# Kernel tuning notes

Hardware: AMD Instinct MI355X
Metric: run time of the kernel (lower is better)

The kernel has to match this reference:

```python
import jax, jax.numpy as jnp
import numpy as np

N, M, DZ, DX, HEADS = 8192, 128, 128, 128, 4


def setup_inputs() -> dict:
    key = jax.random.key(0)
    k1, k2, k3 = jax.random.split(key, 3)
    z = jax.random.normal(k1, (N, DZ), dtype=jnp.float32)
    x = jax.random.normal(k2, (DX, M), dtype=jnp.float32)
    # MLP([input_size, heads]) -> single Linear(DZ+DX, HEADS) + final_act
    W = jax.random.normal(k3, (DZ + DX, HEADS), dtype=jnp.float32) * (1.0 / np.sqrt(DZ + DX))
    b = jnp.zeros((HEADS,), dtype=jnp.float32)
    return {"z": z, "x": x, "W": W, "b": b}


def reference(z, x, W, b):
    # Original: cat([repeat_interleave(z[:,None], M, 1), x.T.repeat(N,1,1)], -1) @ W + b
    # Fused equivalent: split W into the z-part and x-part and broadcast-add.
    dz = z.shape[1]
    zW = jnp.einsum('nd,dh->nh', z, W[:dz])        # [N, H]
    xW = jnp.einsum('dm,dh->mh', x, W[dz:])        # [M, H] (x.T @ W2)
    out = zW[:, None, :] + xW[None, :, :] + b      # [N, M, H]
    return jax.nn.relu(out)
```

## Files before the change

### kernel.cpp

```cpp
#include <hip/hip_runtime.h>
#include <hip/hip_bf16.h>


using bf16 = __hip_bfloat16;

union F4 { float4 v; float f[4]; };

__device__ __forceinline__ int sw(int r) { return r + (r >> 3); }

__global__ void __launch_bounds__(256) gam_fused(
    const float* __restrict__ z, const float* __restrict__ x,
    const float* __restrict__ W, const float* __restrict__ b,
    float* __restrict__ out)
{
    __shared__ float4 Wf[292];
    __shared__ float4 tpart[2][128];
    __shared__ float4 tvec[128];
    __shared__ float4 zw[32];

    const int t   = threadIdx.x;
    const int blk = blockIdx.x;

    const float4* zp = (const float4*)(z + (size_t)blk * 32 * 128);
    F4 a0, a1, a2, a3;
    a0.v = zp[t];
    a1.v = zp[t + 256];
    a2.v = zp[t + 512];
    a3.v = zp[t + 768];

    Wf[sw(t)] = ((const float4*)W)[t];
    __syncthreads();

    {
        const int m    = t & 127;
        const int half = t >> 7;
        const float* xp = x + (size_t)(half * 64) * 128 + m;
        float4 acc = make_float4(0.f, 0.f, 0.f, 0.f);
#pragma unroll
        for (int dd = 0; dd < 64; ++dd) {
            float  xv = xp[dd * 128];
            float4 w  = Wf[sw(128 + half * 64 + dd)];
            acc.x = fmaf(xv, w.x, acc.x);
            acc.y = fmaf(xv, w.y, acc.y);
            acc.z = fmaf(xv, w.z, acc.z);
            acc.w = fmaf(xv, w.w, acc.w);
        }
        tpart[half][m] = acc;
    }

    {
        const int d0 = (t & 31) * 4;
        float4 p0 = make_float4(0.f,0.f,0.f,0.f);
        float4 p1 = make_float4(0.f,0.f,0.f,0.f);
        float4 p2 = make_float4(0.f,0.f,0.f,0.f);
        float4 p3 = make_float4(0.f,0.f,0.f,0.f);
#pragma unroll
        for (int j = 0; j < 4; ++j) {
            float4 w = Wf[sw(d0 + j)];
            p0.x = fmaf(a0.f[j], w.x, p0.x); p0.y = fmaf(a0.f[j], w.y, p0.y);
            p0.z = fmaf(a0.f[j], w.z, p0.z); p0.w = fmaf(a0.f[j], w.w, p0.w);
            p1.x = fmaf(a1.f[j], w.x, p1.x); p1.y = fmaf(a1.f[j], w.y, p1.y);
            p1.z = fmaf(a1.f[j], w.z, p1.z); p1.w = fmaf(a1.f[j], w.w, p1.w);
            p2.x = fmaf(a2.f[j], w.x, p2.x); p2.y = fmaf(a2.f[j], w.y, p2.y);
            p2.z = fmaf(a2.f[j], w.z, p2.z); p2.w = fmaf(a2.f[j], w.w, p2.w);
            p3.x = fmaf(a3.f[j], w.x, p3.x); p3.y = fmaf(a3.f[j], w.y, p3.y);
            p3.z = fmaf(a3.f[j], w.z, p3.z); p3.w = fmaf(a3.f[j], w.w, p3.w);
        }
#pragma unroll
        for (int off = 16; off; off >>= 1) {
            p0.x += __shfl_xor(p0.x, off); p0.y += __shfl_xor(p0.y, off);
            p0.z += __shfl_xor(p0.z, off); p0.w += __shfl_xor(p0.w, off);
            p1.x += __shfl_xor(p1.x, off); p1.y += __shfl_xor(p1.y, off);
            p1.z += __shfl_xor(p1.z, off); p1.w += __shfl_xor(p1.w, off);
            p2.x += __shfl_xor(p2.x, off); p2.y += __shfl_xor(p2.y, off);
            p2.z += __shfl_xor(p2.z, off); p2.w += __shfl_xor(p2.w, off);
            p3.x += __shfl_xor(p3.x, off); p3.y += __shfl_xor(p3.y, off);
            p3.z += __shfl_xor(p3.z, off); p3.w += __shfl_xor(p3.w, off);
        }
        if ((t & 31) == 0) {
            const int r = t >> 5;
            zw[r]      = p0;
            zw[r + 8]  = p1;
            zw[r + 16] = p2;
            zw[r + 24] = p3;
        }
    }
    __syncthreads();

    if (t < 128) {
        float4 bv = *(const float4*)b;
        float4 q0 = tpart[0][t];
        float4 q1 = tpart[1][t];
        float4 tv;
        tv.x = q0.x + q1.x + bv.x;
        tv.y = q0.y + q1.y + bv.y;
        tv.z = q0.z + q1.z + bv.z;
        tv.w = q0.w + q1.w + bv.w;
        tvec[t] = tv;
    }
    __syncthreads();

    {
        const float4 tq = tvec[t & 127];
        float4* op = (float4*)out + (size_t)blk * 4096;
#pragma unroll
        for (int it = 0; it < 16; ++it) {
            const int row = it * 2 + (t >> 7);
            float4 s = zw[row];
            float4 v;
            v.x = fmaxf(tq.x + s.x, 0.f);
            v.y = fmaxf(tq.y + s.y, 0.f);
            v.z = fmaxf(tq.z + s.z, 0.f);
            v.w = fmaxf(tq.w + s.w, 0.f);
            op[it * 256 + t] = v;
        }
    }
}

extern "C" void kernel_launch(void* const* d_in, const int* in_sizes, int n_in,
                              void* d_out, int out_size, void* d_ws, size_t ws_size,
                              hipStream_t stream) {
    const float* z = (const float*)d_in[0];
    const float* x = (const float*)d_in[1];
    const float* W = (const float*)d_in[2];
    const float* b = (const float*)d_in[3];
    float* out = (float*)d_out;
    gam_fused<<<256, 256, 0, stream>>>(z, x, W, b, out);
}
```

Baseline: 69.83 us.

## Split fused kernel into projection stage and broadcast-write stage via workspace

Splits the single fused kernel into two launches. The first computes z@W1 into a workspace over 512 blocks, and only block 0 computes x.T@W2 plus the bias. The second writes the broadcast ReLU output over 1024 blocks. This removes the redundant per-block xW computation, which before ran in all 256 blocks and read all of x each time, and spreads the 16 MB output write across more blocks. The cost is an extra kernel launch and a round trip through global memory between the stages.

```diff
diff --git a/kernel.cpp b/kernel.cpp
--- a/kernel.cpp
+++ b/kernel.cpp
@@ -1,42 +1,61 @@
 #include <hip/hip_runtime.h>
-#include <hip/hip_bf16.h>
 
-
-using bf16 = __hip_bfloat16;
 
 union F4 { float4 v; float f[4]; };
 
 __device__ __forceinline__ int sw(int r) { return r + (r >> 3); }
 
-__global__ void __launch_bounds__(256) gam_fused(
+__global__ void __launch_bounds__(256) gam_stage1(
     const float* __restrict__ z, const float* __restrict__ x,
     const float* __restrict__ W, const float* __restrict__ b,
-    float* __restrict__ out)
+    float4* __restrict__ zw_ws, float4* __restrict__ t_ws)
 {
     __shared__ float4 Wf[292];
     __shared__ float4 tpart[2][128];
-    __shared__ float4 tvec[128];
-    __shared__ float4 zw[32];
 
     const int t   = threadIdx.x;
     const int blk = blockIdx.x;
 
-    const float4* zp = (const float4*)(z + (size_t)blk * 32 * 128);
-    F4 a0, a1, a2, a3;
+    const float4* zp = (const float4*)(z + (size_t)blk * 16 * 128);
+    F4 a0, a1;
     a0.v = zp[t];
     a1.v = zp[t + 256];
-    a2.v = zp[t + 512];
-    a3.v = zp[t + 768];
 
     Wf[sw(t)] = ((const float4*)W)[t];
     __syncthreads();
 
     {
+        const int d0 = (t & 31) * 4;
+        float4 p0 = make_float4(0.f,0.f,0.f,0.f);
+        float4 p1 = make_float4(0.f,0.f,0.f,0.f);
+#pragma unroll
+        for (int j = 0; j < 4; ++j) {
+            float4 w = Wf[sw(d0 + j)];
+            p0.x = fmaf(a0.f[j], w.x, p0.x); p0.y = fmaf(a0.f[j], w.y, p0.y);
+            p0.z = fmaf(a0.f[j], w.z, p0.z); p0.w = fmaf(a0.f[j], w.w, p0.w);
+            p1.x = fmaf(a1.f[j], w.x, p1.x); p1.y = fmaf(a1.f[j], w.y, p1.y);
+            p1.z = fmaf(a1.f[j], w.z, p1.z); p1.w = fmaf(a1.f[j], w.w, p1.w);
+        }
+#pragma unroll
+        for (int off = 16; off; off >>= 1) {
+            p0.x += __shfl_xor(p0.x, off); p0.y += __shfl_xor(p0.y, off);
+            p0.z += __shfl_xor(p0.z, off); p0.w += __shfl_xor(p0.w, off);
+            p1.x += __shfl_xor(p1.x, off); p1.y += __shfl_xor(p1.y, off);
+            p1.z += __shfl_xor(p1.z, off); p1.w += __shfl_xor(p1.w, off);
+        }
+        if ((t & 31) == 0) {
+            const int r = t >> 5;
+            zw_ws[blk * 16 + r]     = p0;
+            zw_ws[blk * 16 + r + 8] = p1;
+        }
+    }
+
+    if (blk == 0) {
         const int m    = t & 127;
         const int half = t >> 7;
         const float* xp = x + (size_t)(half * 64) * 128 + m;
         float4 acc = make_float4(0.f, 0.f, 0.f, 0.f);
-#pragma unroll
+#pragma unroll 8
         for (int dd = 0; dd < 64; ++dd) {
             float  xv = xp[dd * 128];
             float4 w  = Wf[sw(128 + half * 64 + dd)];
@@ -46,74 +65,40 @@
             acc.w = fmaf(xv, w.w, acc.w);
         }
         tpart[half][m] = acc;
-    }
-
-    {
-        const int d0 = (t & 31) * 4;
-        float4 p0 = make_float4(0.f,0.f,0.f,0.f);
-        float4 p1 = make_float4(0.f,0.f,0.f,0.f);
-        float4 p2 = make_float4(0.f,0.f,0.f,0.f);
-        float4 p3 = make_float4(0.f,0.f,0.f,0.f);
-#pragma unroll
-        for (int j = 0; j < 4; ++j) {
-            float4 w = Wf[sw(d0 + j)];
-            p0.x = fmaf(a0.f[j], w.x, p0.x); p0.y = fmaf(a0.f[j], w.y, p0.y);
-            p0.z = fmaf(a0.f[j], w.z, p0.z); p0.w = fmaf(a0.f[j], w.w, p0.w);
-            p1.x = fmaf(a1.f[j], w.x, p1.x); p1.y = fmaf(a1.f[j], w.y, p1.y);
-            p1.z = fmaf(a1.f[j], w.z, p1.z); p1.w = fmaf(a1.f[j], w.w, p1.w);
-            p2.x = fmaf(a2.f[j], w.x, p2.x); p2.y = fmaf(a2.f[j], w.y, p2.y);
-            p2.z = fmaf(a2.f[j], w.z, p2.z); p2.w = fmaf(a2.f[j], w.w, p2.w);
-            p3.x = fmaf(a3.f[j], w.x, p3.x); p3.y = fmaf(a3.f[j], w.y, p3.y);
-            p3.z = fmaf(a3.f[j], w.z, p3.z); p3.w = fmaf(a3.f[j], w.w, p3.w);
-        }
-#pragma unroll
-        for (int off = 16; off; off >>= 1) {
-            p0.x += __shfl_xor(p0.x, off); p0.y += __shfl_xor(p0.y, off);
-            p0.z += __shfl_xor(p0.z, off); p0.w += __shfl_xor(p0.w, off);
-            p1.x += __shfl_xor(p1.x, off); p1.y += __shfl_xor(p1.y, off);
-            p1.z += __shfl_xor(p1.z, off); p1.w += __shfl_xor(p1.w, off);
-            p2.x += __shfl_xor(p2.x, off); p2.y += __shfl_xor(p2.y, off);
-            p2.z += __shfl_xor(p2.z, off); p2.w += __shfl_xor(p2.w, off);
-            p3.x += __shfl_xor(p3.x, off); p3.y += __shfl_xor(p3.y, off);
-            p3.z += __shfl_xor(p3.z, off); p3.w += __shfl_xor(p3.w, off);
-        }
-        if ((t & 31) == 0) {
-            const int r = t >> 5;
-            zw[r]      = p0;
-            zw[r + 8]  = p1;
-            zw[r + 16] = p2;
-            zw[r + 24] = p3;
+        __syncthreads();
+        if (t < 128) {
+            float4 bv = *(const float4*)b;
+            float4 q0 = tpart[0][t];
+            float4 q1 = tpart[1][t];
+            float4 tv;
+            tv.x = q0.x + q1.x + bv.x;
+            tv.y = q0.y + q1.y + bv.y;
+            tv.z = q0.z + q1.z + bv.z;
+            tv.w = q0.w + q1.w + bv.w;
+            t_ws[t] = tv;
         }
     }
-    __syncthreads();
+}
 
-    if (t < 128) {
-        float4 bv = *(const float4*)b;
-        float4 q0 = tpart[0][t];
-        float4 q1 = tpart[1][t];
-        float4 tv;
-        tv.x = q0.x + q1.x + bv.x;
-        tv.y = q0.y + q1.y + bv.y;
-        tv.z = q0.z + q1.z + bv.z;
-        tv.w = q0.w + q1.w + bv.w;
-        tvec[t] = tv;
-    }
-    __syncthreads();
-
-    {
-        const float4 tq = tvec[t & 127];
-        float4* op = (float4*)out + (size_t)blk * 4096;
+__global__ void __launch_bounds__(256) gam_stage2(
+    const float4* __restrict__ zw_ws, const float4* __restrict__ t_ws,
+    float4* __restrict__ out4)
+{
+    const int t   = threadIdx.x;
+    const int blk = blockIdx.x;
+    const float4  tq = t_ws[t & 127];
+    const float4* zb = zw_ws + (size_t)blk * 8;
+    float4* op = out4 + (size_t)blk * 1024;
 #pragma unroll
-        for (int it = 0; it < 16; ++it) {
-            const int row = it * 2 + (t >> 7);
-            float4 s = zw[row];
-            float4 v;
-            v.x = fmaxf(tq.x + s.x, 0.f);
-            v.y = fmaxf(tq.y + s.y, 0.f);
-            v.z = fmaxf(tq.z + s.z, 0.f);
-            v.w = fmaxf(tq.w + s.w, 0.f);
-            op[it * 256 + t] = v;
-        }
+    for (int it = 0; it < 4; ++it) {
+        const int row = it * 2 + (t >> 7);
+        float4 s = zb[row];
+        float4 v;
+        v.x = fmaxf(tq.x + s.x, 0.f);
+        v.y = fmaxf(tq.y + s.y, 0.f);
+        v.z = fmaxf(tq.z + s.z, 0.f);
+        v.w = fmaxf(tq.w + s.w, 0.f);
+        op[it * 256 + t] = v;
     }
 }
 
@@ -124,6 +109,8 @@
     const float* x = (const float*)d_in[1];
     const float* W = (const float*)d_in[2];
     const float* b = (const float*)d_in[3];
-    float* out = (float*)d_out;
-    gam_fused<<<256, 256, 0, stream>>>(z, x, W, b, out);
+    float4* zw_ws = (float4*)d_ws;
+    float4* t_ws  = (float4*)d_ws + 8192;
+    gam_stage1<<<512, 256, 0, stream>>>(z, x, W, b, zw_ws, t_ws);
+    gam_stage2<<<1024, 256, 0, stream>>>(zw_ws, t_ws, (float4*)d_out);
 }
```

New measurement: 70.76 us. Within noise of the previous version (+1.3%).
